# Performance work log

Measured on AMD Instinct MI355X. Metric: run time of the kernel, lower is better.

## Reference

```python
import jax, jax.numpy as jnp
import numpy as np

K = 4096      # codebook_size
D = 256       # emb_dim
DECAY = 0.99
EPS = 1e-05
BETA = 0.25


def setup_inputs() -> dict:
    key = jax.random.key(0)
    k1, k2 = jax.random.split(key)
    z_e = jax.random.normal(k1, (32, 1024, D), dtype=jnp.float32)
    codebook = jax.random.normal(k2, (K, D), dtype=jnp.float32) * 0.05
    ema_cluster_size = jnp.zeros((K,), dtype=jnp.float32)
    ema_embed_sum = jnp.zeros((K, D), dtype=jnp.float32)
    return {"z_e": z_e, "codebook": codebook,
            "ema_cluster_size": ema_cluster_size,
            "ema_embed_sum": ema_embed_sum}


def reference(z_e, codebook, ema_cluster_size, ema_embed_sum):
    lead_shape = z_e.shape[:-1]
    z = z_e.reshape(-1, D)                       # [N, D]
    N = z.shape[0]

    # squared distances: ||z||^2 + ||e||^2 - 2 z e^T   -> [N, K]
    z_sq = jnp.sum(z * z, axis=1, keepdims=True)
    e_sq = jnp.sum(codebook * codebook, axis=1)
    distances = z_sq + e_sq[None, :] - 2.0 * (z @ codebook.T)
    indices = jnp.argmin(distances, axis=1)      # [N]

    z_q = codebook[indices].reshape(z_e.shape)   # gather

    commitment = jnp.mean((z_e - jax.lax.stop_gradient(z_q)) ** 2)
    loss_vq = BETA * commitment
    z_q_st = z_e + jax.lax.stop_gradient(z_q - z_e)  # straight-through

    # EMA statistics (scatter-reduce instead of dense one-hot matmul)
    cluster_size_batch = jax.ops.segment_sum(
        jnp.ones((N,), dtype=z.dtype), indices, num_segments=K)
    embed_sum_batch = jax.ops.segment_sum(z, indices, num_segments=K)

    new_ema_cluster_size = ema_cluster_size * DECAY + (1.0 - DECAY) * cluster_size_batch
    new_ema_embed_sum = ema_embed_sum * DECAY + (1.0 - DECAY) * embed_sum_batch
    n = new_ema_cluster_size + EPS * K
    new_codebook = new_ema_embed_sum / n[:, None]

    avg_probs = cluster_size_batch / N
    perplexity = jnp.exp(-jnp.sum(avg_probs * jnp.log(avg_probs + 1e-12)))

    return (z_q_st, indices.reshape(lead_shape), loss_vq, perplexity,
            new_codebook, new_ema_cluster_size, new_ema_embed_sum)
```

## Files before the change

kernel.cpp:

```cpp
#include <hip/hip_runtime.h>
#include <hip/hip_bf16.h>
#include <math.h>

#define DIM    256
#define KCB    4096
#define NROWS  32768
#define DECAYF 0.99f
#define MARGIN 0.024f

#define OUT_ZQ   0
#define OUT_IDX  8388608
#define OUT_LOSS 8421376
#define OUT_PPL  8421377
#define OUT_CB   8421378
#define OUT_CS   9469954
#define OUT_ES   9474050

#define WS_A2      0u
#define WS_EH      33554432u
#define WS_ZSQ     35651584u
#define WS_ESQ     35782656u
#define WS_P1      35799040u
#define WS_PI      39993344u
#define WS_P2      44187648u
#define WS_IDX     48381952u
#define WS_FLIST   48513024u
#define WS_LIST2   48644096u
#define WS_BASE    48775168u
#define WS_ZERO    48791552u
#define WS_COUNTS  48791552u
#define WS_CURSOR  48807936u
#define WS_FLCNT   48824320u
#define WS_ZEROLEN 32772u

#define WS_SLOT    WS_A2
#define WS_CBT     (WS_A2 + 1048576u)

typedef __attribute__((ext_vector_type(8))) short short8;
typedef __attribute__((ext_vector_type(4))) float f32x4;

#define GLOAD(g, l) __builtin_amdgcn_global_load_lds( \
    (const __attribute__((address_space(1))) unsigned int*)(g), \
    (__attribute__((address_space(3))) unsigned int*)(l), 16, 0, 0)

__device__ __forceinline__ unsigned short f2bf(float x) {
  __hip_bfloat16 h = __float2bfloat16(x);
  return *reinterpret_cast<unsigned short*>(&h);
}

__global__ __launch_bounds__(256) void prep_z(
    const float* __restrict__ z, unsigned short* __restrict__ A2,
    float* __restrict__ z_sq) {
  int gw = (blockIdx.x * 256 + threadIdx.x) >> 6;
  int lane = threadIdx.x & 63;
  float4 v = *(const float4*)(z + (size_t)gw * DIM + lane * 4);
  float x[4] = {v.x, v.y, v.z, v.w};
  unsigned short h[4];
  float ss = 0.f;
#pragma unroll
  for (int i = 0; i < 4; ++i) { ss += x[i] * x[i]; h[i] = f2bf(x[i]); }
  *(ushort4*)(A2 + (size_t)gw * 256 + lane * 4) =
      make_ushort4(h[0], h[1], h[2], h[3]);
#pragma unroll
  for (int off = 32; off > 0; off >>= 1) ss += __shfl_down(ss, off);
  if (lane == 0) z_sq[gw] = ss;
}

__global__ __launch_bounds__(256) void prep_e(
    const float* __restrict__ cb, unsigned short* __restrict__ EH,
    float* __restrict__ e_sq) {
  int gw = (blockIdx.x * 256 + threadIdx.x) >> 6;
  int lane = threadIdx.x & 63;
  float4 v = *(const float4*)(cb + (size_t)gw * DIM + lane * 4);
  float x[4] = {v.x, v.y, v.z, v.w};
  unsigned short h[4];
  float ss = 0.f;
#pragma unroll
  for (int i = 0; i < 4; ++i) { ss += x[i] * x[i]; h[i] = f2bf(x[i]); }
  *(ushort4*)(EH + (size_t)gw * 256 + lane * 4) =
      make_ushort4(h[0], h[1], h[2], h[3]);
#pragma unroll
  for (int off = 32; off > 0; off >>= 1) ss += __shfl_down(ss, off);
  if (lane == 0) e_sq[gw] = ss;
}

__global__ __launch_bounds__(256) void tp_cb(
    const float* __restrict__ cb, float* __restrict__ cbT) {
  __shared__ float tile[32][257];
  int c0 = blockIdx.x * 32;
  int t = threadIdx.x;
  int r = t >> 6, c4 = (t & 63) * 4;
#pragma unroll
  for (int i = 0; i < 8; ++i) {
    float4 v = *(const float4*)(cb + (size_t)(c0 + r + i * 4) * DIM + c4);
    tile[r + i * 4][c4 + 0] = v.x;
    tile[r + i * 4][c4 + 1] = v.y;
    tile[r + i * 4][c4 + 2] = v.z;
    tile[r + i * 4][c4 + 3] = v.w;
  }
  __syncthreads();
  int cs = (t & 7) * 4;
#pragma unroll
  for (int j = 0; j < 8; ++j) {
    int d = (t >> 3) + j * 32;
    float4 w = make_float4(tile[cs][d], tile[cs + 1][d],
                           tile[cs + 2][d], tile[cs + 3][d]);
    *(float4*)(cbT + (size_t)d * KCB + c0 + cs) = w;
  }
}

__global__ __launch_bounds__(256) void dist_mfma(
    const unsigned short* __restrict__ A2, const unsigned short* __restrict__ EH,
    const float* __restrict__ e_sq,
    float* __restrict__ p1, int* __restrict__ pi, float* __restrict__ p2) {
  __shared__ __align__(16) unsigned short sZ[2][128 * 32];
  __shared__ __align__(16) unsigned short sE[2][128 * 32];
  __shared__ float se[128];
  __shared__ float sm1[2][128];
  __shared__ int   smi[2][128];
  __shared__ float sm2[2][128];

  int wgid = blockIdx.x;
  int swz = (wgid & 7) * 1024 + (wgid >> 3);
  int rowp = swz >> 5, colp = swz & 31;
  int brow = rowp * 128, bcol = colp * 128;
  int tid = threadIdx.x;
  int lane = tid & 63, w = tid >> 6;
  int wr = w >> 1, wc = w & 1;
  int rl = lane & 15, k8 = lane >> 4;

  f32x4 acc[4][4] = {};

  const char* gA = (const char*)A2;
  const char* gB = (const char*)EH;
  int r0 = tid >> 2;
  int s_src = (tid & 3) ^ (r0 & 3) ^ ((r0 >> 2) & 3);

#define STAGE(b, ks) do {                                                     \
    _Pragma("unroll")                                                         \
    for (int c = 0; c < 2; ++c) {                                             \
      GLOAD(gA + (size_t)(brow + c * 64 + r0) * 512 + (ks) * 64 + s_src * 16, \
            &sZ[b][c * 2048 + tid * 8]);                                      \
      GLOAD(gB + (size_t)(bcol + c * 64 + r0) * 512 + (ks) * 64 + s_src * 16, \
            &sE[b][c * 2048 + tid * 8]);                                      \
    }                                                                         \
  } while (0)

  if (tid < 128) se[tid] = e_sq[bcol + tid];
  STAGE(0, 0);
  asm volatile("s_waitcnt vmcnt(0)" ::: "memory");
  __syncthreads();

#pragma unroll
  for (int ks = 0; ks < 8; ++ks) {
    int cur = ks & 1;
    if (ks < 7) STAGE(cur ^ 1, ks + 1);
    const unsigned short* za = sZ[cur];
    const unsigned short* ea = sE[cur];
    short8 ef[4], zf[4];
    int sseg = (k8 ^ (rl & 3) ^ ((rl >> 2) & 3)) * 8;
#pragma unroll
    for (int mi = 0; mi < 4; ++mi)
      ef[mi] = *(const short8*)&ea[(wr * 64 + mi * 16 + rl) * 32 + sseg];
#pragma unroll
    for (int ni = 0; ni < 4; ++ni)
      zf[ni] = *(const short8*)&za[(wc * 64 + ni * 16 + rl) * 32 + sseg];
#pragma unroll
    for (int mi = 0; mi < 4; ++mi)
#pragma unroll
      for (int ni = 0; ni < 4; ++ni)
        acc[mi][ni] = __builtin_amdgcn_mfma_f32_16x16x32_bf16(
            ef[mi], zf[ni], acc[mi][ni], 0, 0, 0);
    asm volatile("s_waitcnt vmcnt(0)" ::: "memory");
    __syncthreads();
  }
#undef STAGE

  int cb0 = bcol + wr * 64 + k8 * 4;
  float e2l[4][4];
#pragma unroll
  for (int mi = 0; mi < 4; ++mi)
#pragma unroll
    for (int j = 0; j < 4; ++j)
      e2l[mi][j] = se[wr * 64 + mi * 16 + k8 * 4 + j];

#pragma unroll
  for (int ni = 0; ni < 4; ++ni) {
    float m1 = 1e30f, m2 = 1e30f; int i1 = 0;
#pragma unroll
    for (int mi = 0; mi < 4; ++mi) {
#pragma unroll
      for (int j = 0; j < 4; ++j) {
        float q = e2l[mi][j] - 2.0f * acc[mi][ni][j];
        if (q < m1) { m2 = m1; m1 = q; i1 = cb0 + mi * 16 + j; }
        else if (q < m2) m2 = q;
      }
    }
#pragma unroll
    for (int mk = 16; mk <= 32; mk <<= 1) {
      float v1 = __shfl_xor(m1, mk);
      int   vi = __shfl_xor(i1, mk);
      float v2 = __shfl_xor(m2, mk);
      float hi = fmaxf(m1, v1), lo2 = fminf(m2, v2);
      if (v1 < m1) { m1 = v1; i1 = vi; }
      else if (v1 == m1 && vi < i1) i1 = vi;
      m2 = fminf(hi, lo2);
    }
    if (k8 == 0) {
      int rowl = wc * 64 + ni * 16 + rl;
      sm1[wr][rowl] = m1; smi[wr][rowl] = i1; sm2[wr][rowl] = m2;
    }
  }
  __syncthreads();
  if (tid < 128) {
    float a1 = sm1[0][tid]; int ai = smi[0][tid]; float a2 = sm2[0][tid];
    float b1 = sm1[1][tid]; int bi = smi[1][tid]; float b2 = sm2[1][tid];
    float m1, m2; int i1;
    if (b1 < a1) { m1 = b1; i1 = bi; m2 = fminf(a1, b2); }
    else         { m1 = a1; i1 = ai; m2 = fminf(b1, a2); }
    size_t o = (size_t)colp * NROWS + (brow + tid);
    p1[o] = m1; pi[o] = i1; p2[o] = m2;
  }
}

__global__ __launch_bounds__(256) void merge_kernel(
    const float* __restrict__ p1, const int* __restrict__ pi,
    const float* __restrict__ p2, int* __restrict__ flist,
    int* __restrict__ flcnt, unsigned long long* __restrict__ slot) {
  int r = blockIdx.x * 256 + threadIdx.x;
  float m1 = 1e30f, m2 = 1e30f; int i1 = 0;
  for (int cb = 0; cb < 32; ++cb) {
    size_t o = (size_t)cb * NROWS + r;
    float v1 = p1[o]; int vi = pi[o]; float v2 = p2[o];
    float hi = fmaxf(m1, v1), lo2 = fminf(m2, v2);
    if (v1 < m1) { m1 = v1; i1 = vi; }
    else if (v1 == m1 && vi < i1) i1 = vi;
    m2 = fminf(hi, lo2);
  }
  if (m2 - m1 < MARGIN) {
    slot[r] = ~0ULL;
    int p = atomicAdd(flcnt, 1);
    flist[p] = r;
  } else {
    slot[r] = ((unsigned long long)__float_as_uint(m1) << 32) | (unsigned)i1;
  }
}

__global__ __launch_bounds__(256) void rescore_partial(
    const float* __restrict__ z, const float* __restrict__ cbT,
    const float* __restrict__ z_sq, const float* __restrict__ e_sq,
    const int* __restrict__ flist, const int* __restrict__ flcnt,
    unsigned long long* __restrict__ slot) {
  __shared__ float zs[8][256];
  __shared__ int   rid[8];
  __shared__ float zq[8];
  __shared__ unsigned long long wred[4][8];
  int t = threadIdx.x;
  int lane = t & 63, w = t >> 6;
  int cnt = *flcnt;
  int nitems = ((cnt + 7) >> 3) << 2;
  for (int it = blockIdx.x; it < nitems; it += gridDim.x) {
    int batch = it >> 2, quarter = it & 3;
    __syncthreads();
    if (t < 8) {
      int fi = batch * 8 + t;
      int rr = flist[fi < cnt ? fi : (cnt - 1)];
      rid[t] = rr; zq[t] = z_sq[rr];
    }
    __syncthreads();
    {
      int r8 = t >> 5, d0 = (t & 31) * 8;
      const float* zp = z + (size_t)rid[r8] * DIM + d0;
      *(float4*)&zs[r8][d0] = *(const float4*)(zp);
      *(float4*)&zs[r8][d0 + 4] = *(const float4*)(zp + 4);
    }
    __syncthreads();
    int cbase = quarter * 1024 + t * 4;
    float4 es4 = *(const float4*)(e_sq + cbase);
    float a0[8], a1[8], a2[8], a3[8];
#pragma unroll
    for (int r = 0; r < 8; ++r) { a0[r] = 0.f; a1[r] = 0.f; a2[r] = 0.f; a3[r] = 0.f; }
    for (int d = 0; d < DIM; ++d) {
      float4 e = *(const float4*)(cbT + (size_t)d * KCB + cbase);
#pragma unroll
      for (int r = 0; r < 8; ++r) {
        float zv = zs[r][d];
        a0[r] = fmaf(zv, e.x, a0[r]);
        a1[r] = fmaf(zv, e.y, a1[r]);
        a2[r] = fmaf(zv, e.z, a2[r]);
        a3[r] = fmaf(zv, e.w, a3[r]);
      }
    }
#pragma unroll
    for (int r = 0; r < 8; ++r) {
      float d0 = (zq[r] + es4.x) - 2.0f * a0[r];
      float d1 = (zq[r] + es4.y) - 2.0f * a1[r];
      float d2 = (zq[r] + es4.z) - 2.0f * a2[r];
      float d3 = (zq[r] + es4.w) - 2.0f * a3[r];
      float m = d0; int ci = cbase;
      if (d1 < m) { m = d1; ci = cbase + 1; }
      if (d2 < m) { m = d2; ci = cbase + 2; }
      if (d3 < m) { m = d3; ci = cbase + 3; }
      unsigned long long p =
          ((unsigned long long)__float_as_uint(m) << 32) | (unsigned)ci;
#pragma unroll
      for (int mk = 32; mk >= 1; mk >>= 1) {
        unsigned long long q = __shfl_xor(p, mk);
        if (q < p) p = q;
      }
      if (lane == 0) wred[w][r] = p;
    }
    __syncthreads();
    if (t < 8) {
      unsigned long long m = wred[0][t];
      if (wred[1][t] < m) m = wred[1][t];
      if (wred[2][t] < m) m = wred[2][t];
      if (wred[3][t] < m) m = wred[3][t];
      atomicMin(&slot[rid[t]], m);
    }
  }
}

__global__ __launch_bounds__(256) void gather_kernel(
    const float* __restrict__ z, const float* __restrict__ cb,
    const unsigned long long* __restrict__ slot, int* __restrict__ idx,
    float* __restrict__ out_idxf, float* __restrict__ out_zq,
    int* __restrict__ counts, float* __restrict__ lossp) {
  __shared__ float ls[4];
  int gw = (blockIdx.x * 256 + threadIdx.x) >> 6;
  int lane = threadIdx.x & 63;
  int w = threadIdx.x >> 6;
  int k = (int)(unsigned)(slot[gw] & 0xFFFFFFFFu);
  float4 zq = *(const float4*)(cb + (size_t)k * DIM + lane * 4);
  float4 zv = *(const float4*)(z + (size_t)gw * DIM + lane * 4);
  float4 o;
  o.x = zv.x + (zq.x - zv.x);
  o.y = zv.y + (zq.y - zv.y);
  o.z = zv.z + (zq.z - zv.z);
  o.w = zv.w + (zq.w - zv.w);
  *(float4*)(out_zq + (size_t)gw * DIM + lane * 4) = o;
  float dx = zv.x - zq.x, dy = zv.y - zq.y, dz = zv.z - zq.z, dw = zv.w - zq.w;
  float s = dx * dx + dy * dy + dz * dz + dw * dw;
#pragma unroll
  for (int off = 32; off > 0; off >>= 1) s += __shfl_down(s, off);
  if (lane == 0) {
    ls[w] = s;
    idx[gw] = k;
    out_idxf[gw] = (float)k;
    atomicAdd(&counts[k], 1);
  }
  __syncthreads();
  if (threadIdx.x == 0)
    lossp[blockIdx.x] = ls[0] + ls[1] + ls[2] + ls[3];
}

__global__ void prefix_kernel(const int* __restrict__ counts,
                              int* __restrict__ base, int* __restrict__ cursor) {
  __shared__ int part[256];
  __shared__ int pre[256];
  int t = threadIdx.x;
  int loc[16]; int s = 0;
#pragma unroll
  for (int i = 0; i < 16; ++i) { loc[i] = counts[t * 16 + i]; s += loc[i]; }
  part[t] = s;
  __syncthreads();
  if (t == 0) { int a = 0; for (int i = 0; i < 256; ++i) { pre[i] = a; a += part[i]; } }
  __syncthreads();
  int a = pre[t];
#pragma unroll
  for (int i = 0; i < 16; ++i) { base[t * 16 + i] = a; cursor[t * 16 + i] = a; a += loc[i]; }
}

__global__ void scatter_kernel(const int* __restrict__ idx,
                               int* __restrict__ cursor, int* __restrict__ list2) {
  int n = blockIdx.x * 256 + threadIdx.x;
  int k = idx[n];
  int p = atomicAdd(&cursor[k], 1);
  list2[p] = n;
}

__global__ __launch_bounds__(256) void finalize_codes(
    const float* __restrict__ ema_cs, const float* __restrict__ ema_es,
    const int* __restrict__ counts, const int* __restrict__ base,
    const int* __restrict__ list2, const float* __restrict__ z,
    float* __restrict__ out_cb, float* __restrict__ out_cs,
    float* __restrict__ out_es) {
  int gw = (blockIdx.x * 256 + threadIdx.x) >> 6;
  int lane = threadIdx.x & 63;
  int cnt = counts[gw], b0 = base[gw];
  float sx = 0.f, sy = 0.f, sz = 0.f, sw = 0.f;
  for (int i = 0; i < cnt; ++i) {
    int n = list2[b0 + i];
    float4 v = *(const float4*)(z + (size_t)n * DIM + lane * 4);
    sx += v.x; sy += v.y; sz += v.z; sw += v.w;
  }
  const float omd = 1.0f - DECAYF;
  float cntf = (float)cnt;
  float ncs = ema_cs[gw] * DECAYF + omd * cntf;
  float nden = ncs + 0.04096f;
  if (lane == 0) out_cs[gw] = ncs;
  size_t o = (size_t)gw * DIM + lane * 4;
  float4 em = *(const float4*)(ema_es + o);
  float nex = em.x * DECAYF + omd * sx;
  float ney = em.y * DECAYF + omd * sy;
  float nez = em.z * DECAYF + omd * sz;
  float new_ = em.w * DECAYF + omd * sw;
  *(float2*)(out_es + o) = make_float2(nex, ney);
  *(float2*)(out_es + o + 2) = make_float2(nez, new_);
  *(float2*)(out_cb + o) = make_float2(nex / nden, ney / nden);
  *(float2*)(out_cb + o + 2) = make_float2(nez / nden, new_ / nden);
}

__global__ __launch_bounds__(256) void finalize_scalars(
    const float* __restrict__ lossp, const int* __restrict__ counts,
    float* __restrict__ out_loss, float* __restrict__ out_ppl) {
  __shared__ float red[256];
  int t = threadIdx.x;
  float s = 0.f;
  for (int i = t; i < 8192; i += 256) s += lossp[i];
  float e = 0.f;
  for (int i = t; i < 4096; i += 256) {
    float p = (float)counts[i] * (1.0f / (float)NROWS);
    e -= p * logf(p + 1e-12f);
  }
  red[t] = s;
  __syncthreads();
  for (int st = 128; st > 0; st >>= 1) {
    if (t < st) red[t] += red[t + st];
    __syncthreads();
  }
  float loss_tot = red[0];
  __syncthreads();
  red[t] = e;
  __syncthreads();
  for (int st = 128; st > 0; st >>= 1) {
    if (t < st) red[t] += red[t + st];
    __syncthreads();
  }
  if (t == 0) {
    out_loss[0] = 0.25f * (loss_tot / 8388608.0f);
    out_ppl[0] = expf(red[0]);
  }
}

extern "C" void kernel_launch(void* const* d_in, const int* in_sizes, int n_in,
                              void* d_out, int out_size, void* d_ws, size_t ws_size,
                              hipStream_t stream) {
  (void)in_sizes; (void)n_in; (void)out_size; (void)ws_size;
  const float* z      = (const float*)d_in[0];
  const float* cb     = (const float*)d_in[1];
  const float* ema_cs = (const float*)d_in[2];
  const float* ema_es = (const float*)d_in[3];
  float* out = (float*)d_out;
  char*  ws  = (char*)d_ws;

  unsigned short* A2 = (unsigned short*)(ws + WS_A2);
  unsigned short* EH = (unsigned short*)(ws + WS_EH);
  float* z_sq  = (float*)(ws + WS_ZSQ);
  float* e_sq  = (float*)(ws + WS_ESQ);
  float* p1    = (float*)(ws + WS_P1);
  int*   pi    = (int*)(ws + WS_PI);
  float* p2    = (float*)(ws + WS_P2);
  float* lossp = (float*)(ws + WS_P2);
  unsigned long long* slot = (unsigned long long*)(ws + WS_SLOT);
  float* cbT   = (float*)(ws + WS_CBT);
  int*   idx   = (int*)(ws + WS_IDX);
  int*   flist = (int*)(ws + WS_FLIST);
  int*   list2 = (int*)(ws + WS_LIST2);
  int*   base  = (int*)(ws + WS_BASE);
  int*   counts = (int*)(ws + WS_COUNTS);
  int*   cursor = (int*)(ws + WS_CURSOR);
  int*   flcnt  = (int*)(ws + WS_FLCNT);

  hipMemsetAsync(ws + WS_ZERO, 0, WS_ZEROLEN, stream);

  prep_z<<<NROWS / 4, 256, 0, stream>>>(z, A2, z_sq);
  prep_e<<<KCB / 4, 256, 0, stream>>>(cb, EH, e_sq);
  dist_mfma<<<(NROWS / 128) * (KCB / 128), 256, 0, stream>>>(A2, EH, e_sq,
                                                             p1, pi, p2);
  tp_cb<<<KCB / 32, 256, 0, stream>>>(cb, cbT);
  merge_kernel<<<NROWS / 256, 256, 0, stream>>>(p1, pi, p2, flist, flcnt,
                                                slot);
  rescore_partial<<<2048, 256, 0, stream>>>(z, cbT, z_sq, e_sq, flist, flcnt,
                                            slot);
  gather_kernel<<<NROWS / 4, 256, 0, stream>>>(z, cb, slot, idx,
                                               out + OUT_IDX, out + OUT_ZQ,
                                               counts, lossp);
  prefix_kernel<<<1, 256, 0, stream>>>(counts, base, cursor);
  scatter_kernel<<<NROWS / 256, 256, 0, stream>>>(idx, cursor, list2);
  finalize_codes<<<KCB / 4, 256, 0, stream>>>(ema_cs, ema_es, counts, base,
                                              list2, z, out + OUT_CB,
                                              out + OUT_CS, out + OUT_ES);
  finalize_scalars<<<1, 256, 0, stream>>>(lossp, counts, out + OUT_LOSS,
                                          out + OUT_PPL);
}
```

Baseline: 265.2 us.

## Triple-buffer distance GEMM loads and merge small launches

The distance MFMA kernel moves from double to triple-buffered LDS staging with prefetch depth two. Partial vmcnt waits and a raw s_barrier replace the full drain and __syncthreads on every k-step, so loads can overlap more compute. The two prep kernels are merged into one launch, and the scalar loss/perplexity reduction is folded into block 0 of finalize_codes to drop a launch. The cost is more LDS per block, which may lower occupancy, and block 0 of finalize_codes now does extra serial work.

```diff
diff --git a/kernel.cpp b/kernel.cpp
--- a/kernel.cpp
+++ b/kernel.cpp
@@ -48,40 +48,34 @@
   return *reinterpret_cast<unsigned short*>(&h);
 }
 
-__global__ __launch_bounds__(256) void prep_z(
-    const float* __restrict__ z, unsigned short* __restrict__ A2,
-    float* __restrict__ z_sq) {
-  int gw = (blockIdx.x * 256 + threadIdx.x) >> 6;
+__global__ __launch_bounds__(256) void prep_all(
+    const float* __restrict__ z, const float* __restrict__ cb,
+    unsigned short* __restrict__ A2, unsigned short* __restrict__ EH,
+    float* __restrict__ z_sq, float* __restrict__ e_sq) {
+  int b = blockIdx.x;
   int lane = threadIdx.x & 63;
-  float4 v = *(const float4*)(z + (size_t)gw * DIM + lane * 4);
+  const float* src;
+  unsigned short* dst;
+  float* sq;
+  int gw;
+  if (b < NROWS / 4) {
+    gw = (b * 256 + threadIdx.x) >> 6;
+    src = z; dst = A2; sq = z_sq;
+  } else {
+    gw = ((b - NROWS / 4) * 256 + threadIdx.x) >> 6;
+    src = cb; dst = EH; sq = e_sq;
+  }
+  float4 v = *(const float4*)(src + (size_t)gw * DIM + lane * 4);
   float x[4] = {v.x, v.y, v.z, v.w};
   unsigned short h[4];
   float ss = 0.f;
 #pragma unroll
   for (int i = 0; i < 4; ++i) { ss += x[i] * x[i]; h[i] = f2bf(x[i]); }
-  *(ushort4*)(A2 + (size_t)gw * 256 + lane * 4) =
+  *(ushort4*)(dst + (size_t)gw * 256 + lane * 4) =
       make_ushort4(h[0], h[1], h[2], h[3]);
 #pragma unroll
   for (int off = 32; off > 0; off >>= 1) ss += __shfl_down(ss, off);
-  if (lane == 0) z_sq[gw] = ss;
-}
-
-__global__ __launch_bounds__(256) void prep_e(
-    const float* __restrict__ cb, unsigned short* __restrict__ EH,
-    float* __restrict__ e_sq) {
-  int gw = (blockIdx.x * 256 + threadIdx.x) >> 6;
-  int lane = threadIdx.x & 63;
-  float4 v = *(const float4*)(cb + (size_t)gw * DIM + lane * 4);
-  float x[4] = {v.x, v.y, v.z, v.w};
-  unsigned short h[4];
-  float ss = 0.f;
-#pragma unroll
-  for (int i = 0; i < 4; ++i) { ss += x[i] * x[i]; h[i] = f2bf(x[i]); }
-  *(ushort4*)(EH + (size_t)gw * 256 + lane * 4) =
-      make_ushort4(h[0], h[1], h[2], h[3]);
-#pragma unroll
-  for (int off = 32; off > 0; off >>= 1) ss += __shfl_down(ss, off);
-  if (lane == 0) e_sq[gw] = ss;
+  if (lane == 0) sq[gw] = ss;
 }
 
 __global__ __launch_bounds__(256) void tp_cb(
@@ -113,8 +107,8 @@
     const unsigned short* __restrict__ A2, const unsigned short* __restrict__ EH,
     const float* __restrict__ e_sq,
     float* __restrict__ p1, int* __restrict__ pi, float* __restrict__ p2) {
-  __shared__ __align__(16) unsigned short sZ[2][128 * 32];
-  __shared__ __align__(16) unsigned short sE[2][128 * 32];
+  __shared__ __align__(16) unsigned short sZ[3][128 * 32];
+  __shared__ __align__(16) unsigned short sE[3][128 * 32];
   __shared__ float se[128];
   __shared__ float sm1[2][128];
   __shared__ int   smi[2][128];
@@ -131,32 +125,34 @@
 
   f32x4 acc[4][4] = {};
 
-  const char* gA = (const char*)A2;
-  const char* gB = (const char*)EH;
   int r0 = tid >> 2;
   int s_src = (tid & 3) ^ (r0 & 3) ^ ((r0 >> 2) & 3);
-
-#define STAGE(b, ks) do {                                                     \
-    _Pragma("unroll")                                                         \
-    for (int c = 0; c < 2; ++c) {                                             \
-      GLOAD(gA + (size_t)(brow + c * 64 + r0) * 512 + (ks) * 64 + s_src * 16, \
-            &sZ[b][c * 2048 + tid * 8]);                                      \
-      GLOAD(gB + (size_t)(bcol + c * 64 + r0) * 512 + (ks) * 64 + s_src * 16, \
-            &sE[b][c * 2048 + tid * 8]);                                      \
-    }                                                                         \
+  const char* baseA = (const char*)A2 + (size_t)(brow + r0) * 512 + s_src * 16;
+  const char* baseB = (const char*)EH + (size_t)(bcol + r0) * 512 + s_src * 16;
+
+#define STAGE(b, ks_) do {                                                    \
+    GLOAD(baseA + (ks_) * 64,         &sZ[b][tid * 8]);                       \
+    GLOAD(baseA + 32768 + (ks_) * 64, &sZ[b][2048 + tid * 8]);                \
+    GLOAD(baseB + (ks_) * 64,         &sE[b][tid * 8]);                       \
+    GLOAD(baseB + 32768 + (ks_) * 64, &sE[b][2048 + tid * 8]);                \
   } while (0)
 
   if (tid < 128) se[tid] = e_sq[bcol + tid];
   STAGE(0, 0);
-  asm volatile("s_waitcnt vmcnt(0)" ::: "memory");
+  STAGE(1, 1);
   __syncthreads();
 
 #pragma unroll
   for (int ks = 0; ks < 8; ++ks) {
-    int cur = ks & 1;
-    if (ks < 7) STAGE(cur ^ 1, ks + 1);
-    const unsigned short* za = sZ[cur];
-    const unsigned short* ea = sE[cur];
+    if (ks >= 2 && ks < 7) { asm volatile("s_waitcnt vmcnt(4)" ::: "memory"); }
+    if (ks == 7)           { asm volatile("s_waitcnt vmcnt(0)" ::: "memory"); }
+    if (ks >= 1) {
+      __builtin_amdgcn_sched_barrier(0);
+      __builtin_amdgcn_s_barrier();
+      __builtin_amdgcn_sched_barrier(0);
+    }
+    const unsigned short* za = sZ[ks % 3];
+    const unsigned short* ea = sE[ks % 3];
     short8 ef[4], zf[4];
     int sseg = (k8 ^ (rl & 3) ^ ((rl >> 2) & 3)) * 8;
 #pragma unroll
@@ -171,8 +167,7 @@
       for (int ni = 0; ni < 4; ++ni)
         acc[mi][ni] = __builtin_amdgcn_mfma_f32_16x16x32_bf16(
             ef[mi], zf[ni], acc[mi][ni], 0, 0, 0);
-    asm volatile("s_waitcnt vmcnt(0)" ::: "memory");
-    __syncthreads();
+    if (ks < 6) STAGE((ks + 2) % 3, ks + 2);
   }
 #undef STAGE
 
@@ -384,7 +379,9 @@
     const int* __restrict__ counts, const int* __restrict__ base,
     const int* __restrict__ list2, const float* __restrict__ z,
     float* __restrict__ out_cb, float* __restrict__ out_cs,
-    float* __restrict__ out_es) {
+    float* __restrict__ out_es, const float* __restrict__ lossp,
+    float* __restrict__ out_loss, float* __restrict__ out_ppl) {
+  __shared__ float red[256];
   int gw = (blockIdx.x * 256 + threadIdx.x) >> 6;
   int lane = threadIdx.x & 63;
   int cnt = counts[gw], b0 = base[gw];
@@ -409,37 +406,34 @@
   *(float2*)(out_es + o + 2) = make_float2(nez, new_);
   *(float2*)(out_cb + o) = make_float2(nex / nden, ney / nden);
   *(float2*)(out_cb + o + 2) = make_float2(nez / nden, new_ / nden);
-}
-
-__global__ __launch_bounds__(256) void finalize_scalars(
-    const float* __restrict__ lossp, const int* __restrict__ counts,
-    float* __restrict__ out_loss, float* __restrict__ out_ppl) {
-  __shared__ float red[256];
-  int t = threadIdx.x;
-  float s = 0.f;
-  for (int i = t; i < 8192; i += 256) s += lossp[i];
-  float e = 0.f;
-  for (int i = t; i < 4096; i += 256) {
-    float p = (float)counts[i] * (1.0f / (float)NROWS);
-    e -= p * logf(p + 1e-12f);
-  }
-  red[t] = s;
-  __syncthreads();
-  for (int st = 128; st > 0; st >>= 1) {
-    if (t < st) red[t] += red[t + st];
-    __syncthreads();
-  }
-  float loss_tot = red[0];
-  __syncthreads();
-  red[t] = e;
-  __syncthreads();
-  for (int st = 128; st > 0; st >>= 1) {
-    if (t < st) red[t] += red[t + st];
-    __syncthreads();
-  }
-  if (t == 0) {
-    out_loss[0] = 0.25f * (loss_tot / 8388608.0f);
-    out_ppl[0] = expf(red[0]);
+
+  if (blockIdx.x == 0) {
+    int t = threadIdx.x;
+    float s = 0.f;
+    for (int i = t; i < 8192; i += 256) s += lossp[i];
+    float e = 0.f;
+    for (int i = t; i < 4096; i += 256) {
+      float p = (float)counts[i] * (1.0f / (float)NROWS);
+      e -= p * logf(p + 1e-12f);
+    }
+    red[t] = s;
+    __syncthreads();
+    for (int st = 128; st > 0; st >>= 1) {
+      if (t < st) red[t] += red[t + st];
+      __syncthreads();
+    }
+    float loss_tot = red[0];
+    __syncthreads();
+    red[t] = e;
+    __syncthreads();
+    for (int st = 128; st > 0; st >>= 1) {
+      if (t < st) red[t] += red[t + st];
+      __syncthreads();
+    }
+    if (t == 0) {
+      out_loss[0] = 0.25f * (loss_tot / 8388608.0f);
+      out_ppl[0] = expf(red[0]);
+    }
   }
 }
 
@@ -474,8 +468,7 @@
 
   hipMemsetAsync(ws + WS_ZERO, 0, WS_ZEROLEN, stream);
 
-  prep_z<<<NROWS / 4, 256, 0, stream>>>(z, A2, z_sq);
-  prep_e<<<KCB / 4, 256, 0, stream>>>(cb, EH, e_sq);
+  prep_all<<<NROWS / 4 + KCB / 4, 256, 0, stream>>>(z, cb, A2, EH, z_sq, e_sq);
   dist_mfma<<<(NROWS / 128) * (KCB / 128), 256, 0, stream>>>(A2, EH, e_sq,
                                                              p1, pi, p2);
   tp_cb<<<KCB / 32, 256, 0, stream>>>(cb, cbT);
@@ -490,7 +483,7 @@
   scatter_kernel<<<NROWS / 256, 256, 0, stream>>>(idx, cursor, list2);
   finalize_codes<<<KCB / 4, 256, 0, stream>>>(ema_cs, ema_es, counts, base,
                                               list2, z, out + OUT_CB,
-                                              out + OUT_CS, out + OUT_ES);
-  finalize_scalars<<<1, 256, 0, stream>>>(lossp, counts, out + OUT_LOSS,
-                                          out + OUT_PPL);
-}
+                                              out + OUT_CS, out + OUT_ES,
+                                              lossp, out + OUT_LOSS,
+                                              out + OUT_PPL);
+}
```

Measured after the change: 258.6 us. -2.5%, faster.
